# Optimization experiments

Hardware: AMD Instinct MI355X
Metric: run time of the kernel (lower is better)

## Reference

```python
import jax, jax.numpy as jnp
import numpy as np

N = 50000        # nodes
E = 800000       # edges (avg degree 16)
IN = 128         # n_feat
C0, H0 = 32, 4   # layer0: out_channels, heads (concat -> 128)
C1, H1 = 32, 1   # layer1: out_channels, heads (mean)
NEG_SLOPE = 0.2


def setup_inputs() -> dict:
    key = jax.random.key(0)
    ks = jax.random.split(key, 16)
    def p(k, shape, fan):
        return jax.random.normal(k, shape, jnp.float32) / np.float32(np.sqrt(fan))
    x = jax.random.normal(ks[0], (N, IN), jnp.float32)
    edge_index = jax.random.randint(ks[1], (2, E), 0, N, dtype=jnp.int32)
    return {
        "x": x,
        "edge_index": edge_index,
        # layer 0 GATConv: in=128 -> 4 heads x 32, concat
        "W0": p(ks[2], (H0 * C0, IN), IN),
        "att_src0": p(ks[3], (H0, C0), C0),
        "att_dst0": p(ks[4], (H0, C0), C0),
        "bias0": jnp.zeros((H0 * C0,), jnp.float32),
        "linW0": p(ks[5], (H0 * C0, IN), IN),
        "linb0": jnp.zeros((H0 * C0,), jnp.float32),
        # layer 1 GATConv: in=128 -> 1 head x 32, mean
        "W1": p(ks[6], (H1 * C1, H0 * C0), H0 * C0),
        "att_src1": p(ks[7], (H1, C1), C1),
        "att_dst1": p(ks[8], (H1, C1), C1),
        "bias1": jnp.zeros((C1,), jnp.float32),
        "linW1": p(ks[9], (C1, H0 * C0), H0 * C0),
        "linb1": jnp.zeros((C1,), jnp.float32),
    }


def gat_conv(x, src, dst, W, att_src, att_dst, bias, concat):
    """PyG-style GATConv (self-loops already appended to src/dst)."""
    n = x.shape[0]
    H, C = att_src.shape
    h = (x @ W.T).reshape(n, H, C)                       # [N,H,C]
    a_src = jnp.einsum('nhc,hc->nh', h, att_src)          # [N,H]
    a_dst = jnp.einsum('nhc,hc->nh', h, att_dst)          # [N,H]
    e = jax.nn.leaky_relu(a_src[src] + a_dst[dst], NEG_SLOPE)  # [E,H]
    # segment softmax over incoming edges of each dst node
    m = jax.ops.segment_max(e, dst, num_segments=n)       # [N,H]
    ex = jnp.exp(e - m[dst])
    denom = jax.ops.segment_sum(ex, dst, num_segments=n)  # [N,H]
    alpha = ex / (denom[dst] + 1e-16)                     # [E,H]
    out = jax.ops.segment_sum(h[src] * alpha[:, :, None], dst, num_segments=n)  # [N,H,C]
    out = out.reshape(n, H * C) if concat else out.mean(axis=1)
    return out + bias


def reference(x, edge_index, W0, att_src0, att_dst0, bias0, linW0, linb0,
              W1, att_src1, att_dst1, bias1, linW1, linb1):
    n = x.shape[0]
    loop = jnp.arange(n, dtype=edge_index.dtype)
    src = jnp.concatenate([edge_index[0], loop])  # add self-loops
    dst = jnp.concatenate([edge_index[1], loop])
    # layer 0: conv + linear skip, then ELU (eval mode -> dropout is a no-op)
    h = gat_conv(x, src, dst, W0, att_src0, att_dst0, bias0, True) + x @ linW0.T + linb0
    h = jax.nn.elu(h)
    # layer 1 (last): conv + linear skip, no activation
    out = gat_conv(h, src, dst, W1, att_src1, att_dst1, bias1, False) + h @ linW1.T + linb1
    return out
```

## Files before the change

### kernel.cpp

```cpp
#include <hip/hip_runtime.h>
#include <hip/hip_bf16.h>


typedef __attribute__((ext_vector_type(8))) short bf8_t;
typedef __attribute__((ext_vector_type(4))) float f4_t;
typedef __attribute__((ext_vector_type(2))) float f2_t;

#define NBUCK 256
#define BCAP  8192

__device__ inline short f2bf(float f) {
    return (short)__builtin_bit_cast(unsigned short, __float2bfloat16(f));
}
__device__ inline float blo(unsigned int p) { return __uint_as_float(p << 16); }
__device__ inline float bhi(unsigned int p) { return __uint_as_float(p & 0xffff0000u); }
__device__ inline float lrexp(float e) {
    e = (e > 0.f) ? e : 0.2f * e;
    return __expf(e);
}

__global__ __launch_bounds__(256) void k_initbucket(
    const int* __restrict__ ei,
    const float* __restrict__ W0, const float* __restrict__ lW0,
    const float* __restrict__ W1, const float* __restrict__ lW1,
    const float* __restrict__ b0, const float* __restrict__ lb0,
    const float* __restrict__ b1, const float* __restrict__ lb1,
    short* __restrict__ Wp0, short* __restrict__ lWp0,
    short* __restrict__ Wp1, short* __restrict__ lWp1,
    float* __restrict__ bc0, float* __restrict__ bc1,
    int* __restrict__ gcur,
    unsigned int* __restrict__ bucketed, int E, int T) {
    __shared__ int hist[NBUCK];
    __shared__ int gbase[NBUCK];
    int tid = threadIdx.x;

    if (blockIdx.x < 64) {
        int i = blockIdx.x * 256 + tid;
        {
            int j = i & 7, lane = (i >> 3) & 63, kc = i >> 9;
            int kb = kc & 3, ct = kc >> 2;
            int src = (ct * 16 + (lane & 15)) * 128 + kb * 32 + (lane >> 4) * 8 + j;
            Wp0[i]  = f2bf(W0[src]);
            lWp0[i] = f2bf(lW0[src]);
            if (i < 4096) {
                Wp1[i]  = f2bf(W1[src]);
                lWp1[i] = f2bf(lW1[src]);
            }
        }
        if (i < 128) bc0[i] = b0[i] + lb0[i];
        else if (i < 160) bc1[i - 128] = b1[i - 128] + lb1[i - 128];
        return;
    }

    int bb = blockIdx.x - 64;
    hist[tid] = 0;
    __syncthreads();
    int base = bb * 2048;
    unsigned int pk[8]; int rk[8]; int bk[8];
    #pragma unroll
    for (int j = 0; j < 8; j++) {
        int e = base + j * 256 + tid;
        if (e < T) {
            int src, dst;
            if (e < E) { src = ei[e]; dst = ei[E + e]; }
            else       { src = e - E; dst = src; }
            int b = dst >> 8;
            pk[j] = ((unsigned int)dst << 16) | (unsigned int)src;
            bk[j] = b;
            rk[j] = atomicAdd(&hist[b], 1);
        } else bk[j] = -1;
    }
    __syncthreads();
    int h = hist[tid];
    if (h > 0) gbase[tid] = tid * BCAP + atomicAdd(&gcur[tid], h);
    __syncthreads();
    #pragma unroll
    for (int j = 0; j < 8; j++)
        if (bk[j] >= 0)
            bucketed[gbase[bk[j]] + rk[j]] = pk[j];
}


#define TSTR 136

__global__ __launch_bounds__(256) void k_fillgemm0(
    const unsigned int* __restrict__ bucketed, const int* __restrict__ gcur,
    int* __restrict__ rowstart,
    unsigned short* __restrict__ esrc,
    const float* __restrict__ x,
    const short* __restrict__ Wp0, const short* __restrict__ lWp0,
    const float* __restrict__ as0, const float* __restrict__ ad0,
    unsigned char* __restrict__ h0f8, __hip_bfloat16* __restrict__ skipb,
    float* __restrict__ a0s, float* __restrict__ a0d, int N) {
    __shared__ int ihist[256];
    __shared__ int incl[256];
    __shared__ short tile[4][16 * TSTR];
    __shared__ unsigned char t8[4][16 * 136];
    int NBK = (N + 255) >> 8;

    if ((int)blockIdx.x < NBK) {
        int b = blockIdx.x, t = threadIdx.x;
        int nodebase = b << 8;
        int cntt = gcur[t];
        incl[t] = cntt;
        __syncthreads();
        for (int off = 1; off < 256; off <<= 1) {
            int tv = (t >= off) ? incl[t - off] : 0;
            __syncthreads();
            incl[t] += tv;
            __syncthreads();
        }
        int rbase = (b > 0) ? incl[b - 1] : 0;
        if (b == 0 && t == 255) rowstart[N] = incl[255];
        int used = gcur[b];
        const unsigned int* bk = bucketed + (size_t)b * BCAP;
        __syncthreads();
        ihist[t] = 0;
        __syncthreads();
        for (int i = t; i < used; i += 256)
            atomicAdd(&ihist[(bk[i] >> 16) - nodebase], 1);
        __syncthreads();
        int v = ihist[t];
        incl[t] = v;
        __syncthreads();
        for (int off = 1; off < 256; off <<= 1) {
            int tv = (t >= off) ? incl[t - off] : 0;
            __syncthreads();
            incl[t] += tv;
            __syncthreads();
        }
        int myexcl = incl[t] - v;
        int node = nodebase + t;
        if (node < N) rowstart[node] = rbase + myexcl;
        __syncthreads();
        ihist[t] = myexcl;
        __syncthreads();
        for (int i = t; i < used; i += 256) {
            unsigned int p = bk[i];
            int pos = atomicAdd(&ihist[(p >> 16) - nodebase], 1);
            esrc[rbase + pos] = (unsigned short)(p & 0xffffu);
        }
        return;
    }

    int bx = blockIdx.x - NBK;
    int wv = threadIdx.x >> 6, lane = threadIdx.x & 63;
    int rowbase = bx * 64 + wv * 16;
    int m = lane & 15, q = lane >> 4;
    int arow = rowbase + m; if (arow >= N) arow = N - 1;
    bf8_t a[4];
    #pragma unroll
    for (int kb = 0; kb < 4; kb++) {
        const float4* px = (const float4*)(x + (size_t)arow * 128 + kb * 32 + q * 8);
        float4 lo = px[0], hi = px[1];
        bf8_t f;
        f[0] = f2bf(lo.x); f[1] = f2bf(lo.y); f[2] = f2bf(lo.z); f[3] = f2bf(lo.w);
        f[4] = f2bf(hi.x); f[5] = f2bf(hi.y); f[6] = f2bf(hi.z); f[7] = f2bf(hi.w);
        a[kb] = f;
    }
    float sacc[4][4], dacc[4][4];
    #pragma unroll
    for (int h = 0; h < 4; h++)
        #pragma unroll
        for (int r = 0; r < 4; r++) { sacc[h][r] = 0.f; dacc[h][r] = 0.f; }
    short* tl = tile[wv];
    unsigned char* t8l = t8[wv];
    int r4 = lane >> 2, qt = lane & 3;
    int drow = rowbase + r4;

    #pragma unroll
    for (int ct = 0; ct < 8; ct++) {
        f4_t acc = {0.f, 0.f, 0.f, 0.f};
        #pragma unroll
        for (int kb = 0; kb < 4; kb++) {
            bf8_t b = *(const bf8_t*)(Wp0 + (((ct * 4 + kb) * 64 + lane) << 3));
            acc = __builtin_amdgcn_mfma_f32_16x16x32_bf16(a[kb], b, acc, 0, 0, 0);
        }
        int hd = ct >> 1;
        float ws = as0[ct * 16 + m], wd = ad0[ct * 16 + m];
        #pragma unroll
        for (int r = 0; r < 4; r++) {
            sacc[hd][r] += acc[r] * ws;
            dacc[hd][r] += acc[r] * wd;
            int pk8 = __builtin_amdgcn_cvt_pk_fp8_f32(acc[r], acc[r], 0, false);
            t8l[(q * 4 + r) * 136 + ct * 16 + m] = (unsigned char)(pk8 & 0xff);
        }
    }
    if (drow < N) {
        const unsigned char* sp8 = t8l + r4 * 136 + qt * 32;
        uint2 w0 = ((const uint2*)sp8)[0];
        uint2 w1 = ((const uint2*)sp8)[1];
        uint2 w2 = ((const uint2*)sp8)[2];
        uint2 w3 = ((const uint2*)sp8)[3];
        uint4 o0 = make_uint4(w0.x, w0.y, w1.x, w1.y);
        uint4 o1 = make_uint4(w2.x, w2.y, w3.x, w3.y);
        unsigned char* dst = h0f8 + (size_t)drow * 128 + qt * 32;
        *(uint4*)dst = o0;
        *(uint4*)(dst + 16) = o1;
    }

    #pragma unroll
    for (int ct = 0; ct < 8; ct++) {
        f4_t acc = {0.f, 0.f, 0.f, 0.f};
        #pragma unroll
        for (int kb = 0; kb < 4; kb++) {
            bf8_t b = *(const bf8_t*)(lWp0 + (((ct * 4 + kb) * 64 + lane) << 3));
            acc = __builtin_amdgcn_mfma_f32_16x16x32_bf16(a[kb], b, acc, 0, 0, 0);
        }
        #pragma unroll
        for (int r = 0; r < 4; r++)
            tl[(q * 4 + r) * TSTR + ct * 16 + m] = f2bf(acc[r]);
    }
    if (drow < N) {
        short* dst = (short*)skipb + (size_t)drow * 128 + qt * 32;
        const short* srcp = tl + r4 * TSTR + qt * 32;
        #pragma unroll
        for (int s = 0; s < 4; s++)
            *(uint4*)(dst + s * 8) = *(const uint4*)(srcp + s * 8);
    }

    #pragma unroll
    for (int h = 0; h < 4; h++)
        #pragma unroll
        for (int r = 0; r < 4; r++) {
            float s = sacc[h][r], d = dacc[h][r];
            #pragma unroll
            for (int off = 1; off < 16; off <<= 1) {
                s += __shfl_xor(s, off);
                d += __shfl_xor(d, off);
            }
            sacc[h][r] = s; dacc[h][r] = d;
        }
    if (m < 4) {
        #pragma unroll
        for (int r = 0; r < 4; r++) {
            int row = rowbase + q * 4 + r;
            if (row < N) {
                float sv = (m == 0) ? sacc[0][r] : (m == 1) ? sacc[1][r]
                         : (m == 2) ? sacc[2][r] : sacc[3][r];
                float dv = (m == 0) ? dacc[0][r] : (m == 1) ? dacc[1][r]
                         : (m == 2) ? dacc[2][r] : dacc[3][r];
                a0s[row * 4 + m] = sv;
                a0d[row * 4 + m] = dv;
            }
        }
    }
}


__global__ __launch_bounds__(256) void k_aggfuse(
    const int* __restrict__ rowstart, const unsigned short* __restrict__ esrc,
    const uint2* __restrict__ h0f8,
    const float* __restrict__ a0s, const float* __restrict__ a0d,
    const float* __restrict__ bc0,
    const unsigned int* __restrict__ skip0,
    const short* __restrict__ Wp1, const short* __restrict__ lWp1,
    const float* __restrict__ as1, const float* __restrict__ ad1,
    __hip_bfloat16* __restrict__ h1, float* __restrict__ outskip,
    float* __restrict__ a1s, float* __restrict__ a1d, int n) {
    __shared__ __align__(16) short hrow[16][136];
    __shared__ __align__(16) short th[16 * 40];
    __shared__ __align__(16) float ts[16 * 36];
    __shared__ float satt[2][16], datt[2][16];

    int tid = threadIdx.x;
    int nl = tid >> 4, t = tid & 15, hd = t >> 2;
    int rowbase = blockIdx.x << 4;
    int node = rowbase + nl;

    if (node < n) {
        float ad = a0d[node * 4 + hd];
        int s0 = rowstart[node], s1 = rowstart[node + 1];
        float den = 0.f;
        float acc[8];
        #pragma unroll
        for (int k = 0; k < 8; k++) acc[k] = 0.f;
        int i = s0;
        for (; i + 3 < s1; i += 4) {
            int sE[4]; float e[4]; uint2 p[4];
            #pragma unroll
            for (int j = 0; j < 4; j++) sE[j] = esrc[i + j];
            #pragma unroll
            for (int j = 0; j < 4; j++) e[j] = a0s[sE[j] * 4 + hd] + ad;
            #pragma unroll
            for (int j = 0; j < 4; j++) p[j] = h0f8[(size_t)sE[j] * 16 + t];
            #pragma unroll
            for (int j = 0; j < 4; j++) {
                float wgt = lrexp(e[j]);
                den += wgt;
                f2_t c01 = __builtin_amdgcn_cvt_pk_f32_fp8(p[j].x, false);
                f2_t c23 = __builtin_amdgcn_cvt_pk_f32_fp8(p[j].x, true);
                f2_t c45 = __builtin_amdgcn_cvt_pk_f32_fp8(p[j].y, false);
                f2_t c67 = __builtin_amdgcn_cvt_pk_f32_fp8(p[j].y, true);
                acc[0] += wgt * c01.x; acc[1] += wgt * c01.y;
                acc[2] += wgt * c23.x; acc[3] += wgt * c23.y;
                acc[4] += wgt * c45.x; acc[5] += wgt * c45.y;
                acc[6] += wgt * c67.x; acc[7] += wgt * c67.y;
            }
        }
        for (; i < s1; ++i) {
            int s = esrc[i];
            float wgt = lrexp(a0s[s * 4 + hd] + ad);
            uint2 p = h0f8[(size_t)s * 16 + t];
            den += wgt;
            f2_t c01 = __builtin_amdgcn_cvt_pk_f32_fp8(p.x, false);
            f2_t c23 = __builtin_amdgcn_cvt_pk_f32_fp8(p.x, true);
            f2_t c45 = __builtin_amdgcn_cvt_pk_f32_fp8(p.y, false);
            f2_t c67 = __builtin_amdgcn_cvt_pk_f32_fp8(p.y, true);
            acc[0] += wgt * c01.x; acc[1] += wgt * c01.y;
            acc[2] += wgt * c23.x; acc[3] += wgt * c23.y;
            acc[4] += wgt * c45.x; acc[5] += wgt * c45.y;
            acc[6] += wgt * c67.x; acc[7] += wgt * c67.y;
        }
        float inv = 1.0f / (den + 1e-16f);
        uint4 sp = *(const uint4*)(skip0 + (size_t)node * 64 + t * 4);
        int c0 = t * 8;
        float o[8];
        o[0] = acc[0] * inv + blo(sp.x) + bc0[c0 + 0];
        o[1] = acc[1] * inv + bhi(sp.x) + bc0[c0 + 1];
        o[2] = acc[2] * inv + blo(sp.y) + bc0[c0 + 2];
        o[3] = acc[3] * inv + bhi(sp.y) + bc0[c0 + 3];
        o[4] = acc[4] * inv + blo(sp.z) + bc0[c0 + 4];
        o[5] = acc[5] * inv + bhi(sp.z) + bc0[c0 + 5];
        o[6] = acc[6] * inv + blo(sp.w) + bc0[c0 + 6];
        o[7] = acc[7] * inv + bhi(sp.w) + bc0[c0 + 7];
        #pragma unroll
        for (int k = 0; k < 8; k++)
            o[k] = (o[k] > 0.f) ? o[k] : (__expf(o[k]) - 1.f);
        uint4 res;
        res.x = (unsigned int)(unsigned short)f2bf(o[0]) | ((unsigned int)(unsigned short)f2bf(o[1]) << 16);
        res.y = (unsigned int)(unsigned short)f2bf(o[2]) | ((unsigned int)(unsigned short)f2bf(o[3]) << 16);
        res.z = (unsigned int)(unsigned short)f2bf(o[4]) | ((unsigned int)(unsigned short)f2bf(o[5]) << 16);
        res.w = (unsigned int)(unsigned short)f2bf(o[6]) | ((unsigned int)(unsigned short)f2bf(o[7]) << 16);
        *(uint4*)&hrow[nl][t * 8] = res;
    } else {
        *(uint4*)&hrow[nl][t * 8] = make_uint4(0u, 0u, 0u, 0u);
    }
    __syncthreads();

    int wv = tid >> 6, lane = tid & 63;
    int m = lane & 15, q = lane >> 4;
    bf8_t a[4];
    #pragma unroll
    for (int kb = 0; kb < 4; kb++)
        a[kb] = *(const bf8_t*)&hrow[m][kb * 32 + q * 8];
    int ct = wv & 1;
    const short* Wt = (wv < 2) ? Wp1 : lWp1;
    f4_t acc = {0.f, 0.f, 0.f, 0.f};
    #pragma unroll
    for (int kb = 0; kb < 4; kb++) {
        bf8_t b = *(const bf8_t*)(Wt + (((ct * 4 + kb) * 64 + lane) << 3));
        acc = __builtin_amdgcn_mfma_f32_16x16x32_bf16(a[kb], b, acc, 0, 0, 0);
    }
    if (wv < 2) {
        float wsv = as1[ct * 16 + m], wdv = ad1[ct * 16 + m];
        #pragma unroll
        for (int r = 0; r < 4; r++) {
            th[(q * 4 + r) * 40 + ct * 16 + m] = f2bf(acc[r]);
            float s = acc[r] * wsv, d = acc[r] * wdv;
            #pragma unroll
            for (int off = 1; off < 16; off <<= 1) {
                s += __shfl_xor(s, off);
                d += __shfl_xor(d, off);
            }
            if (m == 0) { satt[ct][q * 4 + r] = s; datt[ct][q * 4 + r] = d; }
        }
    } else {
        #pragma unroll
        for (int r = 0; r < 4; r++)
            ts[(q * 4 + r) * 36 + ct * 16 + m] = acc[r];
    }
    __syncthreads();

    if (tid < 64) {
        int row = tid >> 2, qt = tid & 3;
        if (rowbase + row < n)
            *(uint4*)((short*)h1 + (size_t)(rowbase + row) * 32 + qt * 8) =
                *(const uint4*)&th[row * 40 + qt * 8];
    } else if (tid < 192) {
        int i2 = tid - 64, row = i2 >> 3, qt = i2 & 7;
        if (rowbase + row < n)
            *(uint4*)(outskip + (size_t)(rowbase + row) * 32 + qt * 4) =
                *(const uint4*)&ts[row * 36 + qt * 4];
    } else if (tid < 208) {
        int r2 = tid - 192;
        if (rowbase + r2 < n) {
            a1s[rowbase + r2] = satt[0][r2] + satt[1][r2];
            a1d[rowbase + r2] = datt[0][r2] + datt[1][r2];
        }
    }
}


__global__ __launch_bounds__(256) void k_agg1(
    const int* __restrict__ rowstart, const unsigned short* __restrict__ esrc,
    const __hip_bfloat16* __restrict__ h1,
    const float* __restrict__ a1s, const float* __restrict__ a1d,
    const float* __restrict__ bc1,
    float* __restrict__ out, int n) {
    int node = (blockIdx.x * 256 + threadIdx.x) >> 6;
    int lane = threadIdx.x & 63;
    if (node >= n) return;
    int g = lane >> 4, t = lane & 15;
    float ad = a1d[node];
    int s0 = rowstart[node], s1 = rowstart[node + 1];
    const unsigned int* h1w = (const unsigned int*)h1;
    float den = 0.f, acc0 = 0.f, acc1 = 0.f;
    int i = s0 + g;
    for (; i + 12 < s1; i += 16) {
        int sE[4]; float e[4]; unsigned int p[4];
        #pragma unroll
        for (int j = 0; j < 4; j++) sE[j] = esrc[i + 4 * j];
        #pragma unroll
        for (int j = 0; j < 4; j++) e[j] = a1s[sE[j]] + ad;
        #pragma unroll
        for (int j = 0; j < 4; j++) p[j] = h1w[(size_t)sE[j] * 16 + t];
        #pragma unroll
        for (int j = 0; j < 4; j++) {
            float wgt = lrexp(e[j]);
            den += wgt;
            acc0 += wgt * blo(p[j]);
            acc1 += wgt * bhi(p[j]);
        }
    }
    for (; i < s1; i += 4) {
        int s = esrc[i];
        float wv = lrexp(a1s[s] + ad);
        unsigned int p = h1w[(size_t)s * 16 + t];
        den += wv; acc0 += wv * blo(p); acc1 += wv * bhi(p);
    }
    acc0 += __shfl_xor(acc0, 16); acc0 += __shfl_xor(acc0, 32);
    acc1 += __shfl_xor(acc1, 16); acc1 += __shfl_xor(acc1, 32);
    den  += __shfl_xor(den, 16);  den  += __shfl_xor(den, 32);
    if (g == 0) {
        float inv = 1.0f / (den + 1e-16f);
        int c0 = t * 2;
        size_t idx = (size_t)node * 32 + c0;
        float2 sk = *(const float2*)(out + idx);
        float2 r;
        r.x = acc0 * inv + sk.x + bc1[c0];
        r.y = acc1 * inv + sk.y + bc1[c0 + 1];
        *(float2*)(out + idx) = r;
    }
}


extern "C" void kernel_launch(void* const* d_in, const int* in_sizes, int n_in,
                              void* d_out, int out_size, void* d_ws, size_t ws_size,
                              hipStream_t stream) {
    const float* x   = (const float*)d_in[0];
    const int*   ei  = (const int*)d_in[1];
    const float* W0  = (const float*)d_in[2];
    const float* as0 = (const float*)d_in[3];
    const float* ad0 = (const float*)d_in[4];
    const float* b0  = (const float*)d_in[5];
    const float* lW0 = (const float*)d_in[6];
    const float* lb0 = (const float*)d_in[7];
    const float* W1  = (const float*)d_in[8];
    const float* as1 = (const float*)d_in[9];
    const float* ad1 = (const float*)d_in[10];
    const float* b1  = (const float*)d_in[11];
    const float* lW1 = (const float*)d_in[12];
    const float* lb1 = (const float*)d_in[13];
    float* out = (float*)d_out;

    const int N = in_sizes[0] / 128;
    const int E = in_sizes[1] / 2;
    const int T = E + N;
    const int NBK  = (N + 255) >> 8;
    const int NBBK = (T + 2047) / 2048;

    char* w = (char*)d_ws;
    auto alloc = [&](size_t bytes) -> char* {
        char* p = w; w += (bytes + 255) / 256 * 256; return p;
    };
    int* rowstart  = (int*)alloc((size_t)(N + 1) * 4);
    int* gcur      = (int*)alloc(NBUCK * 4);
    unsigned int* bucketed = (unsigned int*)alloc((size_t)NBUCK * BCAP * 4);
    unsigned short* esrc = (unsigned short*)alloc((size_t)T * 2);
    float* aS      = (float*)alloc((size_t)N * 4 * 4);
    float* aD      = (float*)alloc((size_t)N * 4 * 4);
    char* hbuf     = alloc((size_t)N * 128);
    __hip_bfloat16* skip0 = (__hip_bfloat16*)alloc((size_t)N * 128 * 2);
    __hip_bfloat16* h1buf = (__hip_bfloat16*)alloc((size_t)N * 32 * 2);
    float* aS1     = (float*)alloc((size_t)N * 4);
    float* aD1     = (float*)alloc((size_t)N * 4);
    short* Wp0  = (short*)alloc(16384 * 2);
    short* lWp0 = (short*)alloc(16384 * 2);
    short* Wp1  = (short*)alloc(4096 * 2);
    short* lWp1 = (short*)alloc(4096 * 2);
    float* bc0  = (float*)alloc(128 * 4);
    float* bc1  = (float*)alloc(32 * 4);

    hipMemsetAsync(gcur, 0, NBUCK * sizeof(int), stream);
    k_initbucket<<<64 + NBBK, 256, 0, stream>>>(ei, W0, lW0, W1, lW1,
                                                b0, lb0, b1, lb1,
                                                Wp0, lWp0, Wp1, lWp1, bc0, bc1,
                                                gcur, bucketed, E, T);
    k_fillgemm0<<<NBK + (N + 63) / 64, 256, 0, stream>>>(
        bucketed, gcur, rowstart, esrc,
        x, Wp0, lWp0, as0, ad0, (unsigned char*)hbuf, skip0, aS, aD, N);
    k_aggfuse<<<(N + 15) / 16, 256, 0, stream>>>(
        rowstart, esrc, (const uint2*)hbuf, aS, aD, bc0,
        (const unsigned int*)skip0, Wp1, lWp1, as1, ad1,
        h1buf, out, aS1, aD1, N);
    k_agg1<<<(N + 3) / 4, 256, 0, stream>>>(rowstart, esrc, h1buf,
                                            aS1, aD1, bc1, out, N);
}
```

Baseline: 187.6 us.

## Run layer-0 GEMM alongside edge bucketing and convert W0 on the fly

Moves the layer-0 dense GEMM (projection, skip projection and attention logits) into the same launch as edge bucketing, so the two independent stages overlap. The CSR fill moves into its own kernel that runs after them. The GEMM now reads fp32 W0/lW0 directly and converts them to bf16 inside each wave, which drops the separate pre-pack step for those weights. In exchange, every GEMM wave repeats the weight loads and conversions instead of reading a pre-laid-out bf16 buffer, and the kernel count stays the same.

After: 234.0 us. 1.25x slower.

```diff
diff --git a/kernel.cpp b/kernel.cpp
--- a/kernel.cpp
+++ b/kernel.cpp
@@ -8,6 +8,7 @@
 
 #define NBUCK 256
 #define BCAP  8192
+#define TSTR  136
 
 __device__ inline short f2bf(float f) {
     return (short)__builtin_bit_cast(unsigned short, __float2bfloat16(f));
@@ -18,146 +19,90 @@
     e = (e > 0.f) ? e : 0.2f * e;
     return __expf(e);
 }
-
-__global__ __launch_bounds__(256) void k_initbucket(
+__device__ inline bf8_t pack8(const float* src) {
+    const float4* p4 = (const float4*)src;
+    float4 lo = p4[0], hi = p4[1];
+    bf8_t f;
+    f[0] = f2bf(lo.x); f[1] = f2bf(lo.y); f[2] = f2bf(lo.z); f[3] = f2bf(lo.w);
+    f[4] = f2bf(hi.x); f[5] = f2bf(hi.y); f[6] = f2bf(hi.z); f[7] = f2bf(hi.w);
+    return f;
+}
+
+__global__ __launch_bounds__(256) void k_bg0(
     const int* __restrict__ ei,
+    const float* __restrict__ x,
     const float* __restrict__ W0, const float* __restrict__ lW0,
     const float* __restrict__ W1, const float* __restrict__ lW1,
     const float* __restrict__ b0, const float* __restrict__ lb0,
     const float* __restrict__ b1, const float* __restrict__ lb1,
-    short* __restrict__ Wp0, short* __restrict__ lWp0,
+    const float* __restrict__ as0, const float* __restrict__ ad0,
     short* __restrict__ Wp1, short* __restrict__ lWp1,
     float* __restrict__ bc0, float* __restrict__ bc1,
-    int* __restrict__ gcur,
-    unsigned int* __restrict__ bucketed, int E, int T) {
+    int* __restrict__ gcur, unsigned int* __restrict__ bucketed,
+    unsigned char* __restrict__ h0f8, __hip_bfloat16* __restrict__ skipb,
+    float* __restrict__ a0s, float* __restrict__ a0d,
+    int E, int T, int NBBK, int N) {
     __shared__ int hist[NBUCK];
     __shared__ int gbase[NBUCK];
+    __shared__ short tile[4][16 * TSTR];
+    __shared__ unsigned char t8[4][16 * 136];
     int tid = threadIdx.x;
 
-    if (blockIdx.x < 64) {
-        int i = blockIdx.x * 256 + tid;
+    if ((int)blockIdx.x < NBBK) {
+        int bb = blockIdx.x;
+        hist[tid] = 0;
+        __syncthreads();
+        int base = bb * 2048;
+        unsigned int pk[8]; int rk[8]; int bk[8];
+        #pragma unroll
+        for (int j = 0; j < 8; j++) {
+            int e = base + j * 256 + tid;
+            if (e < T) {
+                int src, dst;
+                if (e < E) { src = ei[e]; dst = ei[E + e]; }
+                else       { src = e - E; dst = src; }
+                int b = dst >> 8;
+                pk[j] = ((unsigned int)dst << 16) | (unsigned int)src;
+                bk[j] = b;
+                rk[j] = atomicAdd(&hist[b], 1);
+            } else bk[j] = -1;
+        }
+        __syncthreads();
+        int h = hist[tid];
+        if (h > 0) gbase[tid] = tid * BCAP + atomicAdd(&gcur[tid], h);
+        __syncthreads();
+        #pragma unroll
+        for (int j = 0; j < 8; j++)
+            if (bk[j] >= 0)
+                bucketed[gbase[bk[j]] + rk[j]] = pk[j];
+        return;
+    }
+
+    if ((int)blockIdx.x < NBBK + 16) {
+        int i = (blockIdx.x - NBBK) * 256 + tid;
         {
             int j = i & 7, lane = (i >> 3) & 63, kc = i >> 9;
             int kb = kc & 3, ct = kc >> 2;
             int src = (ct * 16 + (lane & 15)) * 128 + kb * 32 + (lane >> 4) * 8 + j;
-            Wp0[i]  = f2bf(W0[src]);
-            lWp0[i] = f2bf(lW0[src]);
-            if (i < 4096) {
-                Wp1[i]  = f2bf(W1[src]);
-                lWp1[i] = f2bf(lW1[src]);
-            }
-        }
-        if (i < 128) bc0[i] = b0[i] + lb0[i];
-        else if (i < 160) bc1[i - 128] = b1[i - 128] + lb1[i - 128];
+            Wp1[i]  = f2bf(W1[src]);
+            lWp1[i] = f2bf(lW1[src]);
+        }
+        if (blockIdx.x == (unsigned)NBBK) {
+            if (tid < 128) bc0[tid] = b0[tid] + lb0[tid];
+            else if (tid < 160) bc1[tid - 128] = b1[tid - 128] + lb1[tid - 128];
+        }
         return;
     }
 
-    int bb = blockIdx.x - 64;
-    hist[tid] = 0;
-    __syncthreads();
-    int base = bb * 2048;
-    unsigned int pk[8]; int rk[8]; int bk[8];
-    #pragma unroll
-    for (int j = 0; j < 8; j++) {
-        int e = base + j * 256 + tid;
-        if (e < T) {
-            int src, dst;
-            if (e < E) { src = ei[e]; dst = ei[E + e]; }
-            else       { src = e - E; dst = src; }
-            int b = dst >> 8;
-            pk[j] = ((unsigned int)dst << 16) | (unsigned int)src;
-            bk[j] = b;
-            rk[j] = atomicAdd(&hist[b], 1);
-        } else bk[j] = -1;
-    }
-    __syncthreads();
-    int h = hist[tid];
-    if (h > 0) gbase[tid] = tid * BCAP + atomicAdd(&gcur[tid], h);
-    __syncthreads();
-    #pragma unroll
-    for (int j = 0; j < 8; j++)
-        if (bk[j] >= 0)
-            bucketed[gbase[bk[j]] + rk[j]] = pk[j];
-}
-
-
-#define TSTR 136
-
-__global__ __launch_bounds__(256) void k_fillgemm0(
-    const unsigned int* __restrict__ bucketed, const int* __restrict__ gcur,
-    int* __restrict__ rowstart,
-    unsigned short* __restrict__ esrc,
-    const float* __restrict__ x,
-    const short* __restrict__ Wp0, const short* __restrict__ lWp0,
-    const float* __restrict__ as0, const float* __restrict__ ad0,
-    unsigned char* __restrict__ h0f8, __hip_bfloat16* __restrict__ skipb,
-    float* __restrict__ a0s, float* __restrict__ a0d, int N) {
-    __shared__ int ihist[256];
-    __shared__ int incl[256];
-    __shared__ short tile[4][16 * TSTR];
-    __shared__ unsigned char t8[4][16 * 136];
-    int NBK = (N + 255) >> 8;
-
-    if ((int)blockIdx.x < NBK) {
-        int b = blockIdx.x, t = threadIdx.x;
-        int nodebase = b << 8;
-        int cntt = gcur[t];
-        incl[t] = cntt;
-        __syncthreads();
-        for (int off = 1; off < 256; off <<= 1) {
-            int tv = (t >= off) ? incl[t - off] : 0;
-            __syncthreads();
-            incl[t] += tv;
-            __syncthreads();
-        }
-        int rbase = (b > 0) ? incl[b - 1] : 0;
-        if (b == 0 && t == 255) rowstart[N] = incl[255];
-        int used = gcur[b];
-        const unsigned int* bk = bucketed + (size_t)b * BCAP;
-        __syncthreads();
-        ihist[t] = 0;
-        __syncthreads();
-        for (int i = t; i < used; i += 256)
-            atomicAdd(&ihist[(bk[i] >> 16) - nodebase], 1);
-        __syncthreads();
-        int v = ihist[t];
-        incl[t] = v;
-        __syncthreads();
-        for (int off = 1; off < 256; off <<= 1) {
-            int tv = (t >= off) ? incl[t - off] : 0;
-            __syncthreads();
-            incl[t] += tv;
-            __syncthreads();
-        }
-        int myexcl = incl[t] - v;
-        int node = nodebase + t;
-        if (node < N) rowstart[node] = rbase + myexcl;
-        __syncthreads();
-        ihist[t] = myexcl;
-        __syncthreads();
-        for (int i = t; i < used; i += 256) {
-            unsigned int p = bk[i];
-            int pos = atomicAdd(&ihist[(p >> 16) - nodebase], 1);
-            esrc[rbase + pos] = (unsigned short)(p & 0xffffu);
-        }
-        return;
-    }
-
-    int bx = blockIdx.x - NBK;
-    int wv = threadIdx.x >> 6, lane = threadIdx.x & 63;
+    int bx = blockIdx.x - NBBK - 16;
+    int wv = tid >> 6, lane = tid & 63;
     int rowbase = bx * 64 + wv * 16;
     int m = lane & 15, q = lane >> 4;
     int arow = rowbase + m; if (arow >= N) arow = N - 1;
     bf8_t a[4];
     #pragma unroll
-    for (int kb = 0; kb < 4; kb++) {
-        const float4* px = (const float4*)(x + (size_t)arow * 128 + kb * 32 + q * 8);
-        float4 lo = px[0], hi = px[1];
-        bf8_t f;
-        f[0] = f2bf(lo.x); f[1] = f2bf(lo.y); f[2] = f2bf(lo.z); f[3] = f2bf(lo.w);
-        f[4] = f2bf(hi.x); f[5] = f2bf(hi.y); f[6] = f2bf(hi.z); f[7] = f2bf(hi.w);
-        a[kb] = f;
-    }
+    for (int kb = 0; kb < 4; kb++)
+        a[kb] = pack8(x + (size_t)arow * 128 + kb * 32 + q * 8);
     float sacc[4][4], dacc[4][4];
     #pragma unroll
     for (int h = 0; h < 4; h++)
@@ -167,13 +112,14 @@
     unsigned char* t8l = t8[wv];
     int r4 = lane >> 2, qt = lane & 3;
     int drow = rowbase + r4;
+    int wrow = (lane & 15) * 128 + (lane >> 4) * 8;
 
     #pragma unroll
     for (int ct = 0; ct < 8; ct++) {
         f4_t acc = {0.f, 0.f, 0.f, 0.f};
         #pragma unroll
         for (int kb = 0; kb < 4; kb++) {
-            bf8_t b = *(const bf8_t*)(Wp0 + (((ct * 4 + kb) * 64 + lane) << 3));
+            bf8_t b = pack8(W0 + ct * 16 * 128 + wrow + kb * 32);
             acc = __builtin_amdgcn_mfma_f32_16x16x32_bf16(a[kb], b, acc, 0, 0, 0);
         }
         int hd = ct >> 1;
@@ -204,7 +150,7 @@
         f4_t acc = {0.f, 0.f, 0.f, 0.f};
         #pragma unroll
         for (int kb = 0; kb < 4; kb++) {
-            bf8_t b = *(const bf8_t*)(lWp0 + (((ct * 4 + kb) * 64 + lane) << 3));
+            bf8_t b = pack8(lW0 + ct * 16 * 128 + wrow + kb * 32);
             acc = __builtin_amdgcn_mfma_f32_16x16x32_bf16(a[kb], b, acc, 0, 0, 0);
         }
         #pragma unroll
@@ -247,6 +193,53 @@
     }
 }
 
+__global__ __launch_bounds__(256) void k_fill(
+    const unsigned int* __restrict__ bucketed, const int* __restrict__ gcur,
+    int* __restrict__ rowstart, unsigned short* __restrict__ esrc, int N) {
+    __shared__ int ihist[256];
+    __shared__ int incl[256];
+    int b = blockIdx.x, t = threadIdx.x;
+    int nodebase = b << 8;
+    int cntt = gcur[t];
+    incl[t] = cntt;
+    __syncthreads();
+    for (int off = 1; off < 256; off <<= 1) {
+        int tv = (t >= off) ? incl[t - off] : 0;
+        __syncthreads();
+        incl[t] += tv;
+        __syncthreads();
+    }
+    int rbase = (b > 0) ? incl[b - 1] : 0;
+    if (b == 0 && t == 255) rowstart[N] = incl[255];
+    int used = gcur[b];
+    const unsigned int* bk = bucketed + (size_t)b * BCAP;
+    __syncthreads();
+    ihist[t] = 0;
+    __syncthreads();
+    for (int i = t; i < used; i += 256)
+        atomicAdd(&ihist[(bk[i] >> 16) - nodebase], 1);
+    __syncthreads();
+    int v = ihist[t];
+    incl[t] = v;
+    __syncthreads();
+    for (int off = 1; off < 256; off <<= 1) {
+        int tv = (t >= off) ? incl[t - off] : 0;
+        __syncthreads();
+        incl[t] += tv;
+        __syncthreads();
+    }
+    int myexcl = incl[t] - v;
+    int node = nodebase + t;
+    if (node < N) rowstart[node] = rbase + myexcl;
+    __syncthreads();
+    ihist[t] = myexcl;
+    __syncthreads();
+    for (int i = t; i < used; i += 256) {
+        unsigned int p = bk[i];
+        int pos = atomicAdd(&ihist[(p >> 16) - nodebase], 1);
+        esrc[rbase + pos] = (unsigned short)(p & 0xffffu);
+    }
+}
 
 __global__ __launch_bounds__(256) void k_aggfuse(
     const int* __restrict__ rowstart, const unsigned short* __restrict__ esrc,
@@ -390,7 +383,6 @@
         }
     }
 }
-
 
 __global__ __launch_bounds__(256) void k_agg1(
     const int* __restrict__ rowstart, const unsigned short* __restrict__ esrc,
@@ -469,6 +461,7 @@
     const int T = E + N;
     const int NBK  = (N + 255) >> 8;
     const int NBBK = (T + 2047) / 2048;
+    const int NG0  = (N + 63) / 64;
 
     char* w = (char*)d_ws;
     auto alloc = [&](size_t bytes) -> char* {
@@ -485,21 +478,17 @@
     __hip_bfloat16* h1buf = (__hip_bfloat16*)alloc((size_t)N * 32 * 2);
     float* aS1     = (float*)alloc((size_t)N * 4);
     float* aD1     = (float*)alloc((size_t)N * 4);
-    short* Wp0  = (short*)alloc(16384 * 2);
-    short* lWp0 = (short*)alloc(16384 * 2);
     short* Wp1  = (short*)alloc(4096 * 2);
     short* lWp1 = (short*)alloc(4096 * 2);
     float* bc0  = (float*)alloc(128 * 4);
     float* bc1  = (float*)alloc(32 * 4);
 
     hipMemsetAsync(gcur, 0, NBUCK * sizeof(int), stream);
-    k_initbucket<<<64 + NBBK, 256, 0, stream>>>(ei, W0, lW0, W1, lW1,
-                                                b0, lb0, b1, lb1,
-                                                Wp0, lWp0, Wp1, lWp1, bc0, bc1,
-                                                gcur, bucketed, E, T);
-    k_fillgemm0<<<NBK + (N + 63) / 64, 256, 0, stream>>>(
-        bucketed, gcur, rowstart, esrc,
-        x, Wp0, lWp0, as0, ad0, (unsigned char*)hbuf, skip0, aS, aD, N);
+    k_bg0<<<NBBK + 16 + NG0, 256, 0, stream>>>(
+        ei, x, W0, lW0, W1, lW1, b0, lb0, b1, lb1, as0, ad0,
+        Wp1, lWp1, bc0, bc1, gcur, bucketed,
+        (unsigned char*)hbuf, skip0, aS, aD, E, T, NBBK, N);
+    k_fill<<<NBK, 256, 0, stream>>>(bucketed, gcur, rowstart, esrc, N);
     k_aggfuse<<<(N + 15) / 16, 256, 0, stream>>>(
         rowstart, esrc, (const uint2*)hbuf, aS, aD, bc0,
         (const unsigned int*)skip0, Wp1, lWp1, as1, ad1,
```

## Rebalance kernel stages: overlap edge bucketing with layer-0 GEMM, split CSR fill

Applied to the files above, without the earlier changes.

Regroups the preprocessing kernels. Weight packing and the gcur zeroing now run in a small kernel, which replaces the memset. Edge bucketing and the layer-0 GEMM share one launch, and the CSR fill becomes its own kernel after them. Before, the GEMM waited behind the bucketing kernel. Now the bucketing blocks and the GEMM blocks run concurrently. The cost is one extra kernel launch, with the fill stage serialized after the combined kernel.

New measurement: 198.0 us. +5.6%, slower.

```diff
diff --git a/kernel.cpp b/kernel.cpp
--- a/kernel.cpp
+++ b/kernel.cpp
@@ -8,6 +8,7 @@
 
 #define NBUCK 256
 #define BCAP  8192
+#define TSTR  136
 
 __device__ inline short f2bf(float f) {
     return (short)__builtin_bit_cast(unsigned short, __float2bfloat16(f));
@@ -19,8 +20,7 @@
     return __expf(e);
 }
 
-__global__ __launch_bounds__(256) void k_initbucket(
-    const int* __restrict__ ei,
+__global__ __launch_bounds__(256) void k_pack(
     const float* __restrict__ W0, const float* __restrict__ lW0,
     const float* __restrict__ W1, const float* __restrict__ lW1,
     const float* __restrict__ b0, const float* __restrict__ lb0,
@@ -28,123 +28,72 @@
     short* __restrict__ Wp0, short* __restrict__ lWp0,
     short* __restrict__ Wp1, short* __restrict__ lWp1,
     float* __restrict__ bc0, float* __restrict__ bc1,
-    int* __restrict__ gcur,
-    unsigned int* __restrict__ bucketed, int E, int T) {
-    __shared__ int hist[NBUCK];
-    __shared__ int gbase[NBUCK];
+    int* __restrict__ gcur) {
     int tid = threadIdx.x;
-
-    if (blockIdx.x < 64) {
-        int i = blockIdx.x * 256 + tid;
-        {
-            int j = i & 7, lane = (i >> 3) & 63, kc = i >> 9;
-            int kb = kc & 3, ct = kc >> 2;
-            int src = (ct * 16 + (lane & 15)) * 128 + kb * 32 + (lane >> 4) * 8 + j;
-            Wp0[i]  = f2bf(W0[src]);
-            lWp0[i] = f2bf(lW0[src]);
-            if (i < 4096) {
-                Wp1[i]  = f2bf(W1[src]);
-                lWp1[i] = f2bf(lW1[src]);
-            }
-        }
-        if (i < 128) bc0[i] = b0[i] + lb0[i];
-        else if (i < 160) bc1[i - 128] = b1[i - 128] + lb1[i - 128];
-        return;
-    }
-
-    int bb = blockIdx.x - 64;
-    hist[tid] = 0;
-    __syncthreads();
-    int base = bb * 2048;
-    unsigned int pk[8]; int rk[8]; int bk[8];
-    #pragma unroll
-    for (int j = 0; j < 8; j++) {
-        int e = base + j * 256 + tid;
-        if (e < T) {
-            int src, dst;
-            if (e < E) { src = ei[e]; dst = ei[E + e]; }
-            else       { src = e - E; dst = src; }
-            int b = dst >> 8;
-            pk[j] = ((unsigned int)dst << 16) | (unsigned int)src;
-            bk[j] = b;
-            rk[j] = atomicAdd(&hist[b], 1);
-        } else bk[j] = -1;
-    }
-    __syncthreads();
-    int h = hist[tid];
-    if (h > 0) gbase[tid] = tid * BCAP + atomicAdd(&gcur[tid], h);
-    __syncthreads();
-    #pragma unroll
-    for (int j = 0; j < 8; j++)
-        if (bk[j] >= 0)
-            bucketed[gbase[bk[j]] + rk[j]] = pk[j];
-}
-
-
-#define TSTR 136
-
-__global__ __launch_bounds__(256) void k_fillgemm0(
-    const unsigned int* __restrict__ bucketed, const int* __restrict__ gcur,
-    int* __restrict__ rowstart,
-    unsigned short* __restrict__ esrc,
+    int i = blockIdx.x * 256 + tid;
+    {
+        int j = i & 7, lane = (i >> 3) & 63, kc = i >> 9;
+        int kb = kc & 3, ct = kc >> 2;
+        int src = (ct * 16 + (lane & 15)) * 128 + kb * 32 + (lane >> 4) * 8 + j;
+        Wp0[i]  = f2bf(W0[src]);
+        lWp0[i] = f2bf(lW0[src]);
+        if (i < 4096) {
+            Wp1[i]  = f2bf(W1[src]);
+            lWp1[i] = f2bf(lW1[src]);
+        }
+    }
+    if (blockIdx.x == 0) gcur[tid] = 0;
+    if (i < 128) bc0[i] = b0[i] + lb0[i];
+    else if (i < 160) bc1[i - 128] = b1[i - 128] + lb1[i - 128];
+}
+
+__global__ __launch_bounds__(256) void k_bg(
+    const int* __restrict__ ei,
     const float* __restrict__ x,
     const short* __restrict__ Wp0, const short* __restrict__ lWp0,
     const float* __restrict__ as0, const float* __restrict__ ad0,
+    int* __restrict__ gcur, unsigned int* __restrict__ bucketed,
     unsigned char* __restrict__ h0f8, __hip_bfloat16* __restrict__ skipb,
-    float* __restrict__ a0s, float* __restrict__ a0d, int N) {
-    __shared__ int ihist[256];
-    __shared__ int incl[256];
+    float* __restrict__ a0s, float* __restrict__ a0d,
+    int E, int T, int NBBK, int N) {
+    __shared__ int hist[NBUCK];
+    __shared__ int gbase[NBUCK];
     __shared__ short tile[4][16 * TSTR];
     __shared__ unsigned char t8[4][16 * 136];
-    int NBK = (N + 255) >> 8;
-
-    if ((int)blockIdx.x < NBK) {
-        int b = blockIdx.x, t = threadIdx.x;
-        int nodebase = b << 8;
-        int cntt = gcur[t];
-        incl[t] = cntt;
-        __syncthreads();
-        for (int off = 1; off < 256; off <<= 1) {
-            int tv = (t >= off) ? incl[t - off] : 0;
-            __syncthreads();
-            incl[t] += tv;
-            __syncthreads();
-        }
-        int rbase = (b > 0) ? incl[b - 1] : 0;
-        if (b == 0 && t == 255) rowstart[N] = incl[255];
-        int used = gcur[b];
-        const unsigned int* bk = bucketed + (size_t)b * BCAP;
-        __syncthreads();
-        ihist[t] = 0;
-        __syncthreads();
-        for (int i = t; i < used; i += 256)
-            atomicAdd(&ihist[(bk[i] >> 16) - nodebase], 1);
-        __syncthreads();
-        int v = ihist[t];
-        incl[t] = v;
-        __syncthreads();
-        for (int off = 1; off < 256; off <<= 1) {
-            int tv = (t >= off) ? incl[t - off] : 0;
-            __syncthreads();
-            incl[t] += tv;
-            __syncthreads();
-        }
-        int myexcl = incl[t] - v;
-        int node = nodebase + t;
-        if (node < N) rowstart[node] = rbase + myexcl;
-        __syncthreads();
-        ihist[t] = myexcl;
-        __syncthreads();
-        for (int i = t; i < used; i += 256) {
-            unsigned int p = bk[i];
-            int pos = atomicAdd(&ihist[(p >> 16) - nodebase], 1);
-            esrc[rbase + pos] = (unsigned short)(p & 0xffffu);
-        }
+    int tid = threadIdx.x;
+
+    if ((int)blockIdx.x < NBBK) {
+        int bb = blockIdx.x;
+        hist[tid] = 0;
+        __syncthreads();
+        int base = bb * 2048;
+        unsigned int pk[8]; int rk[8]; int bk[8];
+        #pragma unroll
+        for (int j = 0; j < 8; j++) {
+            int e = base + j * 256 + tid;
+            if (e < T) {
+                int src, dst;
+                if (e < E) { src = ei[e]; dst = ei[E + e]; }
+                else       { src = e - E; dst = src; }
+                int b = dst >> 8;
+                pk[j] = ((unsigned int)dst << 16) | (unsigned int)src;
+                bk[j] = b;
+                rk[j] = atomicAdd(&hist[b], 1);
+            } else bk[j] = -1;
+        }
+        __syncthreads();
+        int h = hist[tid];
+        if (h > 0) gbase[tid] = tid * BCAP + atomicAdd(&gcur[tid], h);
+        __syncthreads();
+        #pragma unroll
+        for (int j = 0; j < 8; j++)
+            if (bk[j] >= 0)
+                bucketed[gbase[bk[j]] + rk[j]] = pk[j];
         return;
     }
 
-    int bx = blockIdx.x - NBK;
-    int wv = threadIdx.x >> 6, lane = threadIdx.x & 63;
+    int bx = blockIdx.x - NBBK;
+    int wv = tid >> 6, lane = tid & 63;
     int rowbase = bx * 64 + wv * 16;
     int m = lane & 15, q = lane >> 4;
     int arow = rowbase + m; if (arow >= N) arow = N - 1;
@@ -247,6 +196,53 @@
     }
 }
 
+__global__ __launch_bounds__(256) void k_fill(
+    const unsigned int* __restrict__ bucketed, const int* __restrict__ gcur,
+    int* __restrict__ rowstart, unsigned short* __restrict__ esrc, int N) {
+    __shared__ int ihist[256];
+    __shared__ int incl[256];
+    int b = blockIdx.x, t = threadIdx.x;
+    int nodebase = b << 8;
+    int cntt = gcur[t];
+    incl[t] = cntt;
+    __syncthreads();
+    for (int off = 1; off < 256; off <<= 1) {
+        int tv = (t >= off) ? incl[t - off] : 0;
+        __syncthreads();
+        incl[t] += tv;
+        __syncthreads();
+    }
+    int rbase = (b > 0) ? incl[b - 1] : 0;
+    if (b == 0 && t == 255) rowstart[N] = incl[255];
+    int used = gcur[b];
+    const unsigned int* bk = bucketed + (size_t)b * BCAP;
+    __syncthreads();
+    ihist[t] = 0;
+    __syncthreads();
+    for (int i = t; i < used; i += 256)
+        atomicAdd(&ihist[(bk[i] >> 16) - nodebase], 1);
+    __syncthreads();
+    int v = ihist[t];
+    incl[t] = v;
+    __syncthreads();
+    for (int off = 1; off < 256; off <<= 1) {
+        int tv = (t >= off) ? incl[t - off] : 0;
+        __syncthreads();
+        incl[t] += tv;
+        __syncthreads();
+    }
+    int myexcl = incl[t] - v;
+    int node = nodebase + t;
+    if (node < N) rowstart[node] = rbase + myexcl;
+    __syncthreads();
+    ihist[t] = myexcl;
+    __syncthreads();
+    for (int i = t; i < used; i += 256) {
+        unsigned int p = bk[i];
+        int pos = atomicAdd(&ihist[(p >> 16) - nodebase], 1);
+        esrc[rbase + pos] = (unsigned short)(p & 0xffffu);
+    }
+}
 
 __global__ __launch_bounds__(256) void k_aggfuse(
     const int* __restrict__ rowstart, const unsigned short* __restrict__ esrc,
@@ -391,7 +387,6 @@
     }
 }
 
-
 __global__ __launch_bounds__(256) void k_agg1(
     const int* __restrict__ rowstart, const unsigned short* __restrict__ esrc,
     const __hip_bfloat16* __restrict__ h1,
@@ -469,6 +464,7 @@
     const int T = E + N;
     const int NBK  = (N + 255) >> 8;
     const int NBBK = (T + 2047) / 2048;
+    const int NG0  = (N + 63) / 64;
 
     char* w = (char*)d_ws;
     auto alloc = [&](size_t bytes) -> char* {
@@ -492,14 +488,12 @@
     float* bc0  = (float*)alloc(128 * 4);
     float* bc1  = (float*)alloc(32 * 4);
 
-    hipMemsetAsync(gcur, 0, NBUCK * sizeof(int), stream);
-    k_initbucket<<<64 + NBBK, 256, 0, stream>>>(ei, W0, lW0, W1, lW1,
-                                                b0, lb0, b1, lb1,
-                                                Wp0, lWp0, Wp1, lWp1, bc0, bc1,
-                                                gcur, bucketed, E, T);
-    k_fillgemm0<<<NBK + (N + 63) / 64, 256, 0, stream>>>(
-        bucketed, gcur, rowstart, esrc,
-        x, Wp0, lWp0, as0, ad0, (unsigned char*)hbuf, skip0, aS, aD, N);
+    k_pack<<<64, 256, 0, stream>>>(W0, lW0, W1, lW1, b0, lb0, b1, lb1,
+                                   Wp0, lWp0, Wp1, lWp1, bc0, bc1, gcur);
+    k_bg<<<NBBK + NG0, 256, 0, stream>>>(
+        ei, x, Wp0, lWp0, as0, ad0, gcur, bucketed,
+        (unsigned char*)hbuf, skip0, aS, aD, E, T, NBBK, N);
+    k_fill<<<NBK, 256, 0, stream>>>(bucketed, gcur, rowstart, esrc, N);
     k_aggfuse<<<(N + 15) / 16, 256, 0, stream>>>(
         rowstart, esrc, (const uint2*)hbuf, aS, aD, bc0,
         (const unsigned int*)skip0, Wp1, lWp1, as1, ad1,
```
